# Optimization experiments

Measured on AMD Instinct MI355X. Metric: run time of the kernel, lower is better.

## Reference

```python
import jax, jax.numpy as jnp
import numpy as np

B = 256   # batch of independent samples (vmap of the module's single-sample forward)
D = 4096  # neurons per topological layer
L = 16    # topological layers -> L-1 edge blocks


def setup_inputs() -> dict:
    key = jax.random.key(0)
    kx, kw, kb = jax.random.split(key, 3)
    x = jax.random.normal(kx, (B, D), dtype=jnp.float32)
    # per-edge scalar weights, batched into dense [D, D] blocks per layer pair
    W = jax.random.normal(kw, (L - 1, D, D), dtype=jnp.float32) * (D ** -0.5)
    # per-neuron biases for all non-input neurons (input neurons' biases are unused in forward)
    b = jax.random.normal(kb, (L - 1, D), dtype=jnp.float32) * 0.1
    return {"x": x, "W": W, "b": b}


def reference(x, W, b):
    """Topo-order DAG evaluation: each neuron = relu(bias + sum_parents w * parent).
    For a layered fully-connected DAG this is exactly a chain of fused GEMM+bias+relu.
    Returns the values of the output-layer neurons, shape [B, D].
    """
    def step(h, wb):
        Wl, bl = wb
        return jax.nn.relu(h @ Wl + bl), None  # [B, D]

    h, _ = jax.lax.scan(step, x, (W, b))
    return h
```

## Files before the change

### kernel.cpp

```cpp
#include <hip/hip_runtime.h>

typedef short short8 __attribute__((ext_vector_type(8)));
typedef float f32x4 __attribute__((ext_vector_type(4)));
typedef unsigned u32x4 __attribute__((ext_vector_type(4)));

#define DD 4096
#define KSL 8
#define KSLAB 512
#define NT 16
#define NLAYER 15

__device__ __forceinline__ unsigned short f2bf(float f) {
  unsigned u = __float_as_uint(f);
  u += 0x7FFFu + ((u >> 16) & 1u);
  return (unsigned short)(u >> 16);
}
__device__ __forceinline__ float bf2f(unsigned short b) {
  return __uint_as_float(((unsigned)b) << 16);
}

__global__ __launch_bounds__(256) void k_tobf16(const float* __restrict__ x,
                                                unsigned short* __restrict__ h) {
  const size_t e = ((size_t)blockIdx.x * 256 + threadIdx.x) * 8;
  const int m = (int)(e >> 12), n = (int)(e & (DD - 1));
  f32x4 a = *(const f32x4*)(x + e);
  f32x4 b = *(const f32x4*)(x + e + 4);
  short8 v;
#pragma unroll
  for (int j = 0; j < 4; ++j) { v[j] = (short)f2bf(a[j]); v[4 + j] = (short)f2bf(b[j]); }
  *(short8*)(h + (size_t)(n >> 5) * 8192 + m * 32 + (n & 31)) = v;
}

__device__ __forceinline__ void qtrans(f32x4 v, int p, unsigned& lo, unsigned& hi) {
  unsigned d0 = (unsigned)f2bf(v[0]) | ((unsigned)f2bf(v[1]) << 16);
  unsigned d1 = (unsigned)f2bf(v[2]) | ((unsigned)f2bf(v[3]) << 16);
  unsigned o0 = (unsigned)__shfl_xor((int)d0, 16);
  unsigned o1 = (unsigned)__shfl_xor((int)d1, 16);
  unsigned r0, r1;
  if ((p & 1) == 0) { r0 = (d0 & 0xFFFFu) | (o0 << 16); r1 = (d0 >> 16) | (o0 & 0xFFFF0000u); }
  else              { r0 = (o1 & 0xFFFFu) | (d1 << 16); r1 = (o1 >> 16) | (d1 & 0xFFFF0000u); }
  unsigned q0 = (unsigned)__shfl_xor((int)r0, 32);
  unsigned q1 = (unsigned)__shfl_xor((int)r1, 32);
  if (p < 2) { lo = r0; hi = q0; } else { lo = q1; hi = r1; }
}

__global__ __launch_bounds__(512, 2) void k_gemm(const unsigned short* __restrict__ A,
                                                 const float* __restrict__ W,
                                                 unsigned short* __restrict__ part) {
  __shared__ __align__(16) unsigned char smem[16384];
  const int bid  = blockIdx.x;
  const int ks   = bid & 7;
  const int nblk = bid >> 3;
  const int n0   = nblk * 128;
  const int tid  = threadIdx.x;
  const int lane = tid & 63;
  const int wave = tid >> 6;
  const int l15  = lane & 15;
  const int p    = lane >> 4;
  const int pp   = ((p & 1) << 1) | (p >> 1);
  const int nw   = 4 * l15 + pp;

  const int kg0 = wave & 3, ns0 = wave >> 2;
  const float* w0 = W + (size_t)(ks * KSLAB + 8 * kg0 + p) * DD + n0 + ns0 * 64 + 4 * l15;

  const int wm = wave & 3, wn = wave >> 2;
  const size_t arow = (size_t)(wm * 64 + l15) * 32 + 8 * p;
  const unsigned short* Ab = A + (size_t)ks * 16 * 8192 + arow;

  const f32x4 fz = {0.f, 0.f, 0.f, 0.f};
  f32x4 acc[4][4];
#pragma unroll
  for (int i = 0; i < 4; ++i)
#pragma unroll
    for (int j = 0; j < 4; ++j) acc[i][j] = fz;

  f32x4 wr[3][2];
  short8 ar[2][4];

#define LOADW(T, S)                                                   \
  do {                                                                \
    const float* s_ = w0 + (size_t)(T) * 32 * DD;                     \
    wr[S][0] = *(const f32x4*)s_;                                     \
    wr[S][1] = *(const f32x4*)(s_ + 4 * DD);                          \
  } while (0)

#define LOADA(T, S)                                                   \
  do {                                                                \
    _Pragma("unroll")                                                 \
    for (int mf = 0; mf < 4; ++mf)                                    \
      ar[S][mf] = *(const short8*)(Ab + (size_t)(T) * 8192 + mf * 16 * 32); \
  } while (0)

#define STAGE(S, BUF)                                                 \
  do {                                                                \
    unsigned la, ha, lb, hb;                                          \
    qtrans(wr[S][0], p, la, ha);                                      \
    qtrans(wr[S][1], p, lb, hb);                                      \
    u32x4 v0 = {la, ha, lb, hb};                                      \
    *(u32x4*)(smem + (BUF) * 8192 + kg0 * 2048 + (ns0 * 64 + nw) * 16) = v0; \
  } while (0)

  LOADW(0, 0);
  LOADW(1, 1);
  LOADW(2, 2);
  LOADA(0, 0);
  STAGE(0, 0);
  __syncthreads();

#pragma unroll
  for (int it = 0; it < NT; ++it) {
    if (it + 1 < NT) LOADA(it + 1, (it + 1) & 1);
    if (it + 1 < NT) STAGE((it + 1) % 3, (it + 1) & 1);
    if (it + 3 < NT) LOADW(it + 3, (it + 3) % 3);
    const unsigned char* bbase = smem + (it & 1) * 8192 + p * 2048 + (wn * 64 + l15) * 16;
#pragma unroll
    for (int nf = 0; nf < 4; ++nf) {
      short8 bf = *(const short8*)(bbase + nf * 256);
#pragma unroll
      for (int mf = 0; mf < 4; ++mf)
        acc[mf][nf] = __builtin_amdgcn_mfma_f32_16x16x32_bf16(ar[it & 1][mf], bf,
                                                              acc[mf][nf], 0, 0, 0);
    }
    __syncthreads();
  }
#undef LOADW
#undef LOADA
#undef STAGE

  unsigned short* pl = part + ((size_t)(ks * 32 + nblk)) * (256 * 128);
#pragma unroll
  for (int mf = 0; mf < 4; ++mf)
#pragma unroll
    for (int nf = 0; nf < 4; ++nf) {
      f32x4 a = acc[mf][nf], o;
#pragma unroll
      for (int j = 0; j < 4; ++j) o[j] = __shfl_xor(a[j], 1);
      if ((l15 & 1) == 0) {
        const int nl = wn * 64 + nf * 16 + l15;
        const int rb = wm * 64 + mf * 16 + 4 * p;
#pragma unroll
        for (int j = 0; j < 4; ++j) {
          unsigned pk = (unsigned)f2bf(a[j]) | ((unsigned)f2bf(o[j]) << 16);
          *(unsigned*)((char*)pl + ((size_t)(rb + j) * 128 + nl) * 2) = pk;
        }
      }
    }
}

__global__ __launch_bounds__(256) void k_reduce(const unsigned short* __restrict__ part,
                                                const float* __restrict__ bias,
                                                unsigned short* __restrict__ hout,
                                                float* __restrict__ fout) {
  const size_t e = ((size_t)blockIdx.x * 256 + threadIdx.x) * 8;
  const int m = (int)(e >> 12), n = (int)(e & (DD - 1));
  const int nblk = n >> 7, nl = n & 127;
  const size_t pofs = ((size_t)nblk * 256 + m) * 128 + nl;
  float s[8] = {0.f, 0.f, 0.f, 0.f, 0.f, 0.f, 0.f, 0.f};
#pragma unroll
  for (int ks = 0; ks < KSL; ++ks) {
    short8 v = *(const short8*)(part + (size_t)ks * (32 * 256 * 128) + pofs);
#pragma unroll
    for (int j = 0; j < 8; ++j) s[j] += bf2f((unsigned short)v[j]);
  }
  f32x4 b0 = *(const f32x4*)(bias + n);
  f32x4 b1 = *(const f32x4*)(bias + n + 4);
#pragma unroll
  for (int j = 0; j < 4; ++j) {
    s[j]     = fmaxf(s[j] + b0[j], 0.f);
    s[4 + j] = fmaxf(s[4 + j] + b1[j], 0.f);
  }
  short8 o;
#pragma unroll
  for (int j = 0; j < 8; ++j) o[j] = (short)f2bf(s[j]);
  *(short8*)(hout + (size_t)(n >> 5) * 8192 + m * 32 + (n & 31)) = o;
  if (fout) {
    f32x4 o0, o1;
#pragma unroll
    for (int j = 0; j < 4; ++j) { o0[j] = s[j]; o1[j] = s[4 + j]; }
    float* dst = fout + e;
    *(f32x4*)dst = o0;
    *(f32x4*)(dst + 4) = o1;
  }
}

extern "C" void kernel_launch(void* const* d_in, const int* in_sizes, int n_in,
                              void* d_out, int out_size, void* d_ws, size_t ws_size,
                              hipStream_t stream) {
  const float* x = (const float*)d_in[0];
  const float* W = (const float*)d_in[1];
  const float* b = (const float*)d_in[2];
  float* out = (float*)d_out;

  char* ws = (char*)d_ws;
  unsigned short* h0 = (unsigned short*)ws;
  unsigned short* h1 = (unsigned short*)(ws + (1 << 21));
  unsigned short* part = (unsigned short*)(ws + (1 << 22));

  k_tobf16<<<512, 256, 0, stream>>>(x, h0);
  unsigned short* hc = h0;
  unsigned short* hn = h1;
  for (int l = 0; l < NLAYER; ++l) {
    const bool last = (l == NLAYER - 1);
    k_gemm<<<256, 512, 0, stream>>>(hc, W + (size_t)l * DD * DD, part);
    k_reduce<<<512, 256, 0, stream>>>(part, b + (size_t)l * DD, hn,
                                      last ? out : nullptr);
    unsigned short* t = hc; hc = hn; hn = t;
  }
}
```

Before: 436.5 us.

## Split GEMM blocks along M into two 128-row halves with 256-thread blocks

Each GEMM block now covers 128 batch rows instead of all 256. It runs 4 waves instead of 8, and the grid grows to 512 blocks with launch bounds of 256 threads and 3 blocks per CU. Each wave now computes a 32x128 tile instead of 64x64 and stages both 64-column halves of the W slab into shared memory. The partial-sum layout and the reduce indexing change to match. The aim is more blocks and better CU fill across the 256 CUs. The cost is that every W slab is read and converted to bf16 twice, once per M half, which doubles W global traffic on an already bandwidth-heavy fp32 weight stream.

```diff
diff --git a/kernel.cpp b/kernel.cpp
--- a/kernel.cpp
+++ b/kernel.cpp
@@ -44,51 +44,53 @@
   if (p < 2) { lo = r0; hi = q0; } else { lo = q1; hi = r1; }
 }
 
-__global__ __launch_bounds__(512, 2) void k_gemm(const unsigned short* __restrict__ A,
+__global__ __launch_bounds__(256, 3) void k_gemm(const unsigned short* __restrict__ A,
                                                  const float* __restrict__ W,
                                                  unsigned short* __restrict__ part) {
   __shared__ __align__(16) unsigned char smem[16384];
   const int bid  = blockIdx.x;
   const int ks   = bid & 7;
-  const int nblk = bid >> 3;
+  const int nblk = (bid >> 3) & 31;
+  const int mb   = bid >> 8;
   const int n0   = nblk * 128;
   const int tid  = threadIdx.x;
   const int lane = tid & 63;
-  const int wave = tid >> 6;
+  const int w    = tid >> 6;
   const int l15  = lane & 15;
   const int p    = lane >> 4;
   const int pp   = ((p & 1) << 1) | (p >> 1);
   const int nw   = 4 * l15 + pp;
 
-  const int kg0 = wave & 3, ns0 = wave >> 2;
-  const float* w0 = W + (size_t)(ks * KSLAB + 8 * kg0 + p) * DD + n0 + ns0 * 64 + 4 * l15;
-
-  const int wm = wave & 3, wn = wave >> 2;
-  const size_t arow = (size_t)(wm * 64 + l15) * 32 + 8 * p;
+  const float* w0 = W + (size_t)(ks * KSLAB + 8 * w + p) * DD + n0 + 4 * l15;
+  const float* w1 = w0 + 64;
+
+  const size_t arow = (size_t)(mb * 128 + w * 32 + l15) * 32 + 8 * p;
   const unsigned short* Ab = A + (size_t)ks * 16 * 8192 + arow;
 
   const f32x4 fz = {0.f, 0.f, 0.f, 0.f};
-  f32x4 acc[4][4];
-#pragma unroll
-  for (int i = 0; i < 4; ++i)
-#pragma unroll
-    for (int j = 0; j < 4; ++j) acc[i][j] = fz;
-
-  f32x4 wr[3][2];
-  short8 ar[2][4];
+  f32x4 acc[2][8];
+#pragma unroll
+  for (int i = 0; i < 2; ++i)
+#pragma unroll
+    for (int j = 0; j < 8; ++j) acc[i][j] = fz;
+
+  f32x4 wr[3][4];
+  short8 ar[2][2];
 
 #define LOADW(T, S)                                                   \
   do {                                                                \
-    const float* s_ = w0 + (size_t)(T) * 32 * DD;                     \
-    wr[S][0] = *(const f32x4*)s_;                                     \
-    wr[S][1] = *(const f32x4*)(s_ + 4 * DD);                          \
+    const float* a_ = w0 + (size_t)(T) * 32 * DD;                     \
+    const float* b_ = w1 + (size_t)(T) * 32 * DD;                     \
+    wr[S][0] = *(const f32x4*)a_;                                     \
+    wr[S][1] = *(const f32x4*)(a_ + 4 * DD);                          \
+    wr[S][2] = *(const f32x4*)b_;                                     \
+    wr[S][3] = *(const f32x4*)(b_ + 4 * DD);                          \
   } while (0)
 
 #define LOADA(T, S)                                                   \
   do {                                                                \
-    _Pragma("unroll")                                                 \
-    for (int mf = 0; mf < 4; ++mf)                                    \
-      ar[S][mf] = *(const short8*)(Ab + (size_t)(T) * 8192 + mf * 16 * 32); \
+    ar[S][0] = *(const short8*)(Ab + (size_t)(T) * 8192);             \
+    ar[S][1] = *(const short8*)(Ab + (size_t)(T) * 8192 + 512);       \
   } while (0)
 
 #define STAGE(S, BUF)                                                 \
@@ -97,7 +99,11 @@
     qtrans(wr[S][0], p, la, ha);                                      \
     qtrans(wr[S][1], p, lb, hb);                                      \
     u32x4 v0 = {la, ha, lb, hb};                                      \
-    *(u32x4*)(smem + (BUF) * 8192 + kg0 * 2048 + (ns0 * 64 + nw) * 16) = v0; \
+    *(u32x4*)(smem + (BUF) * 8192 + w * 2048 + nw * 16) = v0;         \
+    qtrans(wr[S][2], p, la, ha);                                      \
+    qtrans(wr[S][3], p, lb, hb);                                      \
+    u32x4 v1 = {la, ha, lb, hb};                                      \
+    *(u32x4*)(smem + (BUF) * 8192 + w * 2048 + (64 + nw) * 16) = v1;  \
   } while (0)
 
   LOADW(0, 0);
@@ -112,12 +118,12 @@
     if (it + 1 < NT) LOADA(it + 1, (it + 1) & 1);
     if (it + 1 < NT) STAGE((it + 1) % 3, (it + 1) & 1);
     if (it + 3 < NT) LOADW(it + 3, (it + 3) % 3);
-    const unsigned char* bbase = smem + (it & 1) * 8192 + p * 2048 + (wn * 64 + l15) * 16;
-#pragma unroll
-    for (int nf = 0; nf < 4; ++nf) {
-      short8 bf = *(const short8*)(bbase + nf * 256);
-#pragma unroll
-      for (int mf = 0; mf < 4; ++mf)
+    const unsigned char* cb = smem + (it & 1) * 8192 + p * 2048 + l15 * 16;
+#pragma unroll
+    for (int nf = 0; nf < 8; ++nf) {
+      short8 bf = *(const short8*)(cb + nf * 256);
+#pragma unroll
+      for (int mf = 0; mf < 2; ++mf)
         acc[mf][nf] = __builtin_amdgcn_mfma_f32_16x16x32_bf16(ar[it & 1][mf], bf,
                                                               acc[mf][nf], 0, 0, 0);
     }
@@ -127,17 +133,17 @@
 #undef LOADA
 #undef STAGE
 
-  unsigned short* pl = part + ((size_t)(ks * 32 + nblk)) * (256 * 128);
-#pragma unroll
-  for (int mf = 0; mf < 4; ++mf)
-#pragma unroll
-    for (int nf = 0; nf < 4; ++nf) {
+  unsigned short* pl = part + ((size_t)ks << 20) + (size_t)(mb * 32 + nblk) * 16384;
+#pragma unroll
+  for (int mf = 0; mf < 2; ++mf)
+#pragma unroll
+    for (int nf = 0; nf < 8; ++nf) {
       f32x4 a = acc[mf][nf], o;
 #pragma unroll
       for (int j = 0; j < 4; ++j) o[j] = __shfl_xor(a[j], 1);
       if ((l15 & 1) == 0) {
-        const int nl = wn * 64 + nf * 16 + l15;
-        const int rb = wm * 64 + mf * 16 + 4 * p;
+        const int nl = nf * 16 + l15;
+        const int rb = w * 32 + mf * 16 + 4 * p;
 #pragma unroll
         for (int j = 0; j < 4; ++j) {
           unsigned pk = (unsigned)f2bf(a[j]) | ((unsigned)f2bf(o[j]) << 16);
@@ -154,11 +160,12 @@
   const size_t e = ((size_t)blockIdx.x * 256 + threadIdx.x) * 8;
   const int m = (int)(e >> 12), n = (int)(e & (DD - 1));
   const int nblk = n >> 7, nl = n & 127;
-  const size_t pofs = ((size_t)nblk * 256 + m) * 128 + nl;
+  const int mb = m >> 7, ml = m & 127;
+  const size_t pofs = (size_t)(mb * 32 + nblk) * 16384 + ml * 128 + nl;
   float s[8] = {0.f, 0.f, 0.f, 0.f, 0.f, 0.f, 0.f, 0.f};
 #pragma unroll
   for (int ks = 0; ks < KSL; ++ks) {
-    short8 v = *(const short8*)(part + (size_t)ks * (32 * 256 * 128) + pofs);
+    short8 v = *(const short8*)(part + ((size_t)ks << 20) + pofs);
 #pragma unroll
     for (int j = 0; j < 8; ++j) s[j] += bf2f((unsigned short)v[j]);
   }
@@ -201,7 +208,7 @@
   unsigned short* hn = h1;
   for (int l = 0; l < NLAYER; ++l) {
     const bool last = (l == NLAYER - 1);
-    k_gemm<<<256, 512, 0, stream>>>(hc, W + (size_t)l * DD * DD, part);
+    k_gemm<<<512, 256, 0, stream>>>(hc, W + (size_t)l * DD * DD, part);
     k_reduce<<<512, 256, 0, stream>>>(part, b + (size_t)l * DD, hn,
                                       last ? out : nullptr);
     unsigned short* t = hc; hc = hn; hn = t;
```

Result: slower. 463.7 us (+6.2%).
